# Kernel optimization log

Measured on AMD Instinct MI355X. Metric: run time of the kernel, lower is better.

The kernel has to match this reference:

```python
import jax, jax.numpy as jnp
import numpy as np

SIGMA_LIST = [0.05, 0.1, 0.2]
WEIGHT_LIST = [0.3, 0.3, 0.4]


def setup_inputs() -> dict:
    key = jax.random.key(0)
    k1, k2, k3 = jax.random.split(key, 3)
    B, N, M, D, C = 1, 8192, 8192, 3, 16
    x = jax.random.uniform(k1, (B, N, D), dtype=jnp.float32)
    y = jax.random.uniform(k2, (B, M, D), dtype=jnp.float32)
    y_fea = jax.random.normal(k3, (B, M, C), dtype=jnp.float32)
    return {"x": x, "y": y, "y_fea": y_fea}


def reference(x, y, y_fea):
    x2 = jnp.sum(x * x, axis=-1)  # [B, N]
    y2 = jnp.sum(y * y, axis=-1)  # [B, M]
    xy = jnp.einsum("bnd,bmd->bnm", x, y)  # [B, N, M]
    d2 = jnp.maximum(x2[:, :, None] + y2[:, None, :] - 2.0 * xy, 0.0)
    out = jnp.zeros(x.shape[:2] + (y_fea.shape[-1],), dtype=y_fea.dtype)
    for sigma, w in zip(SIGMA_LIST, WEIGHT_LIST):
        k = jnp.exp(d2 * (-1.0 / (2.0 * sigma * sigma)))  # [B, N, M]
        k = k / jnp.sum(k, axis=-1, keepdims=True)  # row-normalize over neighbors
        out = out + w * jnp.einsum("bnm,bmc->bnc", k, y_fea)
    return out
```

## Files before the change

kernel.cpp:

```cpp
#include <hip/hip_runtime.h>


static constexpr int Nn = 8192;
static constexpr int Mm = 8192;
static constexpr int NCH = 8;
static constexpr int NKT = 256 / NCH;
static constexpr float KC = 36.0673761f;
static constexpr float KD = -18.0336880f;

typedef _Float16 half8 __attribute__((ext_vector_type(8)));
typedef __fp16  fp16x2 __attribute__((ext_vector_type(2)));
typedef float  float4v __attribute__((ext_vector_type(4)));

#define MFMA_F16 __builtin_amdgcn_mfma_f32_16x16x32_f16
#define EXP2F(v) __builtin_amdgcn_exp2f(v)

__global__ __launch_bounds__(256) void mgsc_prep(
    const float* __restrict__ y, const float* __restrict__ yf,
    float4* __restrict__ q, _Float16* __restrict__ frag)
{
    const int t = blockIdx.x * 256 + threadIdx.x;
    const int m = t >> 4, c = t & 15;
    const int idx = ((m >> 5) << 9) + ((((m & 31) >> 3) << 4) + c) * 8 + (m & 7);
    frag[idx] = (_Float16)yf[t];
    if (t < Mm) {
        const float ax = y[3 * t], ay = y[3 * t + 1], az = y[3 * t + 2];
        q[t] = make_float4(KC * ax, KC * ay, KC * az,
                           KD * (ax * ax + ay * ay + az * az));
    }
}

__global__ __launch_bounds__(256, 4) void mgsc_main(
    const float* __restrict__ x, const float4* __restrict__ q,
    const _Float16* __restrict__ frag, float* __restrict__ part)
{
    __shared__ float4 qS[NKT * 32];

    const int tid  = threadIdx.x;
    const int wave = tid >> 6, lane = tid & 63;
    const int g    = lane >> 4, c = lane & 15;
    const int xb   = blockIdx.x, yb = blockIdx.y;
    const int n0   = (xb * 4 + wave) * 16;
    const int nrow = n0 + c;

    const float4* qsrc = q + ((size_t)yb * NKT << 5);
#pragma unroll
    for (int i = 0; i < NKT * 32 / 256; ++i)
        qS[tid + 256 * i] = qsrc[tid + 256 * i];

    const float xx = x[3 * nrow], xy = x[3 * nrow + 1], xz = x[3 * nrow + 2];
    const float E2x = EXP2F(KD * __fmaf_rn(xx, xx, __fmaf_rn(xy, xy, xz * xz)));

    float4v acc0 = {0.f, 0.f, 0.f, 0.f}, acc1 = acc0, acc2 = acc0;
    float4v dac0 = acc0, dac1 = acc0, dac2 = acc0;

    const _Float16 onev = (c == 0) ? (_Float16)1.0f : (_Float16)0.0f;
    half8 bone = {onev, onev, onev, onev, onev, onev, onev, onev};

    __syncthreads();

    const _Float16* fp = frag + ((size_t)yb * NKT << 9) + (lane << 3);
    half8 Bc = *reinterpret_cast<const half8*>(fp);

    for (int ktl = 0; ktl < NKT; ++ktl) {
        half8 Bn;
        if (ktl + 1 < NKT) {
            fp += 512;
            Bn = *reinterpret_cast<const half8*>(fp);
        }
        const float4* qk = &qS[(ktl << 5) + (g << 3)];
        float E2[8];
#pragma unroll
        for (int j = 0; j < 8; ++j) {
            const float4 Q = qk[j];
            const float arg = __fmaf_rn(xx, Q.x,
                              __fmaf_rn(xy, Q.y,
                              __fmaf_rn(xz, Q.z, Q.w)));
            E2[j] = E2x * EXP2F(arg);
        }
        union { fp16x2 h2[4]; half8 v; } A2, A1, A0;
#pragma unroll
        for (int jj = 0; jj < 4; ++jj) {
            A2.h2[jj] = __builtin_amdgcn_cvt_pkrtz(E2[2 * jj], E2[2 * jj + 1]);
            const fp16x2 s2 = A2.h2[jj] * A2.h2[jj];
            A1.h2[jj] = s2 * s2;
            const fp16x2 s1 = A1.h2[jj] * A1.h2[jj];
            A0.h2[jj] = s1 * s1;
        }
        acc0 = MFMA_F16(A0.v, Bc, acc0, 0, 0, 0);
        acc1 = MFMA_F16(A1.v, Bc, acc1, 0, 0, 0);
        acc2 = MFMA_F16(A2.v, Bc, acc2, 0, 0, 0);
        dac0 = MFMA_F16(A0.v, bone, dac0, 0, 0, 0);
        dac1 = MFMA_F16(A1.v, bone, dac1, 0, 0, 0);
        dac2 = MFMA_F16(A2.v, bone, dac2, 0, 0, 0);
        if (ktl + 1 < NKT) Bc = Bn;
    }

    float* pb = part + ((size_t)yb * Nn) * 52;
#pragma unroll
    for (int r = 0; r < 4; ++r) {
        const int n = n0 + (g << 2) + r;
        float* row = pb + (size_t)n * 52;
        row[c]      = acc0[r];
        row[16 + c] = acc1[r];
        row[32 + c] = acc2[r];
        if (c == 0) {
            row[48] = dac0[r];
            row[49] = dac1[r];
            row[50] = dac2[r];
        }
    }
}

__global__ __launch_bounds__(256) void mgsc_reduce(
    const float* __restrict__ part, float* __restrict__ out)
{
    const int t = blockIdx.x * 256 + threadIdx.x;
    const int n = t >> 4, c = t & 15;
    float s0 = 0.f, s1 = 0.f, s2 = 0.f, d0 = 0.f, d1 = 0.f, d2 = 0.f;
#pragma unroll
    for (int k = 0; k < NCH; ++k) {
        const float* row = part + ((size_t)k * Nn + n) * 52;
        s0 += row[c];
        s1 += row[16 + c];
        s2 += row[32 + c];
        d0 += row[48];
        d1 += row[49];
        d2 += row[50];
    }
    out[(size_t)n * 16 + c] = 0.3f * s0 / d0 + 0.3f * s1 / d1 + 0.4f * s2 / d2;
}

__global__ __launch_bounds__(256) void mgsc_fused(
    const float* __restrict__ x, const float* __restrict__ y,
    const float* __restrict__ yf, float* __restrict__ out)
{
    __shared__ float yS[256 * 3];
    __shared__ float yfS[256 * 16];
    const int tid = threadIdx.x;
    const int n   = blockIdx.x * 256 + tid;
    const float xx = x[3 * n], xy = x[3 * n + 1], xz = x[3 * n + 2];
    float a0[16], a1[16], a2[16];
#pragma unroll
    for (int c = 0; c < 16; ++c) { a0[c] = 0.f; a1[c] = 0.f; a2[c] = 0.f; }
    float den0 = 0.f, den1 = 0.f, den2 = 0.f;
    for (int mt = 0; mt < Mm; mt += 256) {
        const float4* ysrc = reinterpret_cast<const float4*>(y + (size_t)mt * 3);
        if (tid < 192) reinterpret_cast<float4*>(yS)[tid] = ysrc[tid];
        const float4* fsrc = reinterpret_cast<const float4*>(yf + (size_t)mt * 16);
#pragma unroll
        for (int k = 0; k < 4; ++k)
            reinterpret_cast<float4*>(yfS)[tid + 256 * k] = fsrc[tid + 256 * k];
        __syncthreads();
        for (int mm = 0; mm < 256; ++mm) {
            const float dx = xx - yS[3 * mm], dy = xy - yS[3 * mm + 1], dz = xz - yS[3 * mm + 2];
            const float d2 = dx * dx + dy * dy + dz * dz;
            const float e2 = __expf(-12.5f * d2);
            const float t = e2 * e2, e1 = t * t, u = e1 * e1, e0 = u * u;
            den0 += e0; den1 += e1; den2 += e2;
            const float4* fr = reinterpret_cast<const float4*>(yfS + mm * 16);
#pragma unroll
            for (int k = 0; k < 4; ++k) {
                const float4 f = fr[k];
                a0[4*k+0] += e0 * f.x; a0[4*k+1] += e0 * f.y; a0[4*k+2] += e0 * f.z; a0[4*k+3] += e0 * f.w;
                a1[4*k+0] += e1 * f.x; a1[4*k+1] += e1 * f.y; a1[4*k+2] += e1 * f.z; a1[4*k+3] += e1 * f.w;
                a2[4*k+0] += e2 * f.x; a2[4*k+1] += e2 * f.y; a2[4*k+2] += e2 * f.z; a2[4*k+3] += e2 * f.w;
            }
        }
        __syncthreads();
    }
    const float r0 = 0.3f / den0, r1 = 0.3f / den1, r2 = 0.4f / den2;
#pragma unroll
    for (int c = 0; c < 16; ++c)
        out[(size_t)n * 16 + c] = a0[c] * r0 + a1[c] * r1 + a2[c] * r2;
}

extern "C" void kernel_launch(void* const* d_in, const int* in_sizes, int n_in,
                              void* d_out, int out_size, void* d_ws, size_t ws_size,
                              hipStream_t stream) {
    const float* x  = (const float*)d_in[0];
    const float* y  = (const float*)d_in[1];
    const float* yf = (const float*)d_in[2];
    float* out = (float*)d_out;

    const size_t qB    = (size_t)Mm * sizeof(float4);
    const size_t fragB = (size_t)Mm * 16 * sizeof(_Float16);
    const size_t partB = (size_t)NCH * Nn * 52 * sizeof(float);
    if (qB + fragB + partB > ws_size) {
        mgsc_fused<<<Nn / 256, 256, 0, stream>>>(x, y, yf, out);
        return;
    }
    float4*   q    = (float4*)d_ws;
    _Float16* frag = (_Float16*)((char*)d_ws + qB);
    float*    part = (float*)((char*)d_ws + qB + fragB);

    mgsc_prep<<<(Mm * 16) / 256, 256, 0, stream>>>(y, yf, q, frag);
    mgsc_main<<<dim3(Nn / 64, NCH), 256, 0, stream>>>(x, q, frag, part);
    mgsc_reduce<<<(Nn * 16) / 256, 256, 0, stream>>>(part, out);
}
```

Before: 88.66 us.

## Process two 16-row tiles per wave to reuse B fragments, double M-chunks

Each wave now computes two 16-row x tiles (32 rows), so each loaded y_fea fragment and each LDS q read feed twice as many MFMAs and exp evaluations. The grid is halved along N and the number of M-chunks (NCH) is doubled to 16, which keeps the block count about the same and halves the K length per block. Costs: twice the accumulator registers, which may lower occupancy, and twice the partial-sum buffer that the reduce kernel must read.

```diff
diff --git a/kernel.cpp b/kernel.cpp
--- a/kernel.cpp
+++ b/kernel.cpp
@@ -3,13 +3,15 @@
 
 static constexpr int Nn = 8192;
 static constexpr int Mm = 8192;
-static constexpr int NCH = 8;
+static constexpr int NCH = 16;
 static constexpr int NKT = 256 / NCH;
 static constexpr float KC = 36.0673761f;
 static constexpr float KD = -18.0336880f;
 
 typedef _Float16 half8 __attribute__((ext_vector_type(8)));
 typedef __fp16  fp16x2 __attribute__((ext_vector_type(2)));
+typedef __fp16  fp16x4 __attribute__((ext_vector_type(4)));
+typedef __fp16  fp16x8 __attribute__((ext_vector_type(8)));
 typedef float  float4v __attribute__((ext_vector_type(4)));
 
 #define MFMA_F16 __builtin_amdgcn_mfma_f32_16x16x32_f16
@@ -30,6 +32,36 @@
     }
 }
 
+struct Frags { half8 a0, a1, a2; };
+__device__ __forceinline__ Frags make_frags(const float E[8]) {
+    fp16x2 p[4], q1[4], q0[4];
+#pragma unroll
+    for (int jj = 0; jj < 4; ++jj) {
+        p[jj] = __builtin_amdgcn_cvt_pkrtz(E[2 * jj], E[2 * jj + 1]);
+        const fp16x2 s2 = p[jj] * p[jj];
+        q1[jj] = s2 * s2;
+        const fp16x2 s1 = q1[jj] * q1[jj];
+        q0[jj] = s1 * s1;
+    }
+    Frags f;
+    {
+        const fp16x4 lo = __builtin_shufflevector(p[0], p[1], 0, 1, 2, 3);
+        const fp16x4 hi = __builtin_shufflevector(p[2], p[3], 0, 1, 2, 3);
+        f.a2 = __builtin_bit_cast(half8, __builtin_shufflevector(lo, hi, 0, 1, 2, 3, 4, 5, 6, 7));
+    }
+    {
+        const fp16x4 lo = __builtin_shufflevector(q1[0], q1[1], 0, 1, 2, 3);
+        const fp16x4 hi = __builtin_shufflevector(q1[2], q1[3], 0, 1, 2, 3);
+        f.a1 = __builtin_bit_cast(half8, __builtin_shufflevector(lo, hi, 0, 1, 2, 3, 4, 5, 6, 7));
+    }
+    {
+        const fp16x4 lo = __builtin_shufflevector(q0[0], q0[1], 0, 1, 2, 3);
+        const fp16x4 hi = __builtin_shufflevector(q0[2], q0[3], 0, 1, 2, 3);
+        f.a0 = __builtin_bit_cast(half8, __builtin_shufflevector(lo, hi, 0, 1, 2, 3, 4, 5, 6, 7));
+    }
+    return f;
+}
+
 __global__ __launch_bounds__(256, 4) void mgsc_main(
     const float* __restrict__ x, const float4* __restrict__ q,
     const _Float16* __restrict__ frag, float* __restrict__ part)
@@ -40,75 +72,80 @@
     const int wave = tid >> 6, lane = tid & 63;
     const int g    = lane >> 4, c = lane & 15;
     const int xb   = blockIdx.x, yb = blockIdx.y;
-    const int n0   = (xb * 4 + wave) * 16;
-    const int nrow = n0 + c;
+    const int n0   = (xb * 4 + wave) * 32;
+    const int rA   = n0 + c;
+    const int rB   = n0 + 16 + c;
 
     const float4* qsrc = q + ((size_t)yb * NKT << 5);
-#pragma unroll
-    for (int i = 0; i < NKT * 32 / 256; ++i)
-        qS[tid + 256 * i] = qsrc[tid + 256 * i];
-
-    const float xx = x[3 * nrow], xy = x[3 * nrow + 1], xz = x[3 * nrow + 2];
-    const float E2x = EXP2F(KD * __fmaf_rn(xx, xx, __fmaf_rn(xy, xy, xz * xz)));
-
-    float4v acc0 = {0.f, 0.f, 0.f, 0.f}, acc1 = acc0, acc2 = acc0;
-    float4v dac0 = acc0, dac1 = acc0, dac2 = acc0;
+    qS[tid]       = qsrc[tid];
+    qS[tid + 256] = qsrc[tid + 256];
+
+    const float xxA = x[3 * rA], xyA = x[3 * rA + 1], xzA = x[3 * rA + 2];
+    const float xxB = x[3 * rB], xyB = x[3 * rB + 1], xzB = x[3 * rB + 2];
+    const float E2xA = EXP2F(KD * __fmaf_rn(xxA, xxA, __fmaf_rn(xyA, xyA, xzA * xzA)));
+    const float E2xB = EXP2F(KD * __fmaf_rn(xxB, xxB, __fmaf_rn(xyB, xyB, xzB * xzB)));
+
+    float4v aA0 = {0.f, 0.f, 0.f, 0.f}, aA1 = aA0, aA2 = aA0;
+    float4v dA0 = aA0, dA1 = aA0, dA2 = aA0;
+    float4v aB0 = aA0, aB1 = aA0, aB2 = aA0;
+    float4v dB0 = aA0, dB1 = aA0, dB2 = aA0;
 
     const _Float16 onev = (c == 0) ? (_Float16)1.0f : (_Float16)0.0f;
     half8 bone = {onev, onev, onev, onev, onev, onev, onev, onev};
 
     __syncthreads();
 
-    const _Float16* fp = frag + ((size_t)yb * NKT << 9) + (lane << 3);
-    half8 Bc = *reinterpret_cast<const half8*>(fp);
+    const _Float16* fpp = frag + ((size_t)yb * NKT << 9) + (lane << 3);
+    half8 Bc = *reinterpret_cast<const half8*>(fpp);
 
     for (int ktl = 0; ktl < NKT; ++ktl) {
         half8 Bn;
         if (ktl + 1 < NKT) {
-            fp += 512;
-            Bn = *reinterpret_cast<const half8*>(fp);
+            fpp += 512;
+            Bn = *reinterpret_cast<const half8*>(fpp);
         }
         const float4* qk = &qS[(ktl << 5) + (g << 3)];
-        float E2[8];
+        float EA[8], EB[8];
 #pragma unroll
         for (int j = 0; j < 8; ++j) {
             const float4 Q = qk[j];
-            const float arg = __fmaf_rn(xx, Q.x,
-                              __fmaf_rn(xy, Q.y,
-                              __fmaf_rn(xz, Q.z, Q.w)));
-            E2[j] = E2x * EXP2F(arg);
+            const float argA = __fmaf_rn(xxA, Q.x, __fmaf_rn(xyA, Q.y, __fmaf_rn(xzA, Q.z, Q.w)));
+            const float argB = __fmaf_rn(xxB, Q.x, __fmaf_rn(xyB, Q.y, __fmaf_rn(xzB, Q.z, Q.w)));
+            EA[j] = E2xA * EXP2F(argA);
+            EB[j] = E2xB * EXP2F(argB);
         }
-        union { fp16x2 h2[4]; half8 v; } A2, A1, A0;
-#pragma unroll
-        for (int jj = 0; jj < 4; ++jj) {
-            A2.h2[jj] = __builtin_amdgcn_cvt_pkrtz(E2[2 * jj], E2[2 * jj + 1]);
-            const fp16x2 s2 = A2.h2[jj] * A2.h2[jj];
-            A1.h2[jj] = s2 * s2;
-            const fp16x2 s1 = A1.h2[jj] * A1.h2[jj];
-            A0.h2[jj] = s1 * s1;
-        }
-        acc0 = MFMA_F16(A0.v, Bc, acc0, 0, 0, 0);
-        acc1 = MFMA_F16(A1.v, Bc, acc1, 0, 0, 0);
-        acc2 = MFMA_F16(A2.v, Bc, acc2, 0, 0, 0);
-        dac0 = MFMA_F16(A0.v, bone, dac0, 0, 0, 0);
-        dac1 = MFMA_F16(A1.v, bone, dac1, 0, 0, 0);
-        dac2 = MFMA_F16(A2.v, bone, dac2, 0, 0, 0);
+        const Frags fA = make_frags(EA);
+        const Frags fB = make_frags(EB);
+        aA0 = MFMA_F16(fA.a0, Bc, aA0, 0, 0, 0);
+        aA1 = MFMA_F16(fA.a1, Bc, aA1, 0, 0, 0);
+        aA2 = MFMA_F16(fA.a2, Bc, aA2, 0, 0, 0);
+        dA0 = MFMA_F16(fA.a0, bone, dA0, 0, 0, 0);
+        dA1 = MFMA_F16(fA.a1, bone, dA1, 0, 0, 0);
+        dA2 = MFMA_F16(fA.a2, bone, dA2, 0, 0, 0);
+        aB0 = MFMA_F16(fB.a0, Bc, aB0, 0, 0, 0);
+        aB1 = MFMA_F16(fB.a1, Bc, aB1, 0, 0, 0);
+        aB2 = MFMA_F16(fB.a2, Bc, aB2, 0, 0, 0);
+        dB0 = MFMA_F16(fB.a0, bone, dB0, 0, 0, 0);
+        dB1 = MFMA_F16(fB.a1, bone, dB1, 0, 0, 0);
+        dB2 = MFMA_F16(fB.a2, bone, dB2, 0, 0, 0);
         if (ktl + 1 < NKT) Bc = Bn;
     }
 
     float* pb = part + ((size_t)yb * Nn) * 52;
 #pragma unroll
     for (int r = 0; r < 4; ++r) {
-        const int n = n0 + (g << 2) + r;
-        float* row = pb + (size_t)n * 52;
-        row[c]      = acc0[r];
-        row[16 + c] = acc1[r];
-        row[32 + c] = acc2[r];
-        if (c == 0) {
-            row[48] = dac0[r];
-            row[49] = dac1[r];
-            row[50] = dac2[r];
-        }
+        const int nA = n0 + (g << 2) + r;
+        float* rowA = pb + (size_t)nA * 52;
+        rowA[c]      = aA0[r];
+        rowA[16 + c] = aA1[r];
+        rowA[32 + c] = aA2[r];
+        if (c == 0) { rowA[48] = dA0[r]; rowA[49] = dA1[r]; rowA[50] = dA2[r]; }
+        const int nB = n0 + 16 + (g << 2) + r;
+        float* rowB = pb + (size_t)nB * 52;
+        rowB[c]      = aB0[r];
+        rowB[16 + c] = aB1[r];
+        rowB[32 + c] = aB2[r];
+        if (c == 0) { rowB[48] = dB0[r]; rowB[49] = dB1[r]; rowB[50] = dB2[r]; }
     }
 }
 
@@ -195,6 +232,6 @@
     float*    part = (float*)((char*)d_ws + qB + fragB);
 
     mgsc_prep<<<(Mm * 16) / 256, 256, 0, stream>>>(y, yf, q, frag);
-    mgsc_main<<<dim3(Nn / 64, NCH), 256, 0, stream>>>(x, q, frag, part);
+    mgsc_main<<<dim3(Nn / 128, NCH), 256, 0, stream>>>(x, q, frag, part);
     mgsc_reduce<<<(Nn * 16) / 256, 256, 0, stream>>>(part, out);
 }
```

Result: slower. 93.43 us (+5.4%).

## Fuse prep kernel into main by staging y and features into LDS per block

Applied to the files above, without the earlier changes.

Removes the separate prep launch. Each main block now computes its own scaled y coordinates (stored structure-of-arrays in LDS) and converts its chunk of features to fp16 MFMA fragment layout in LDS. The B operand is then read from LDS each iteration instead of being prefetched from global memory. This saves one kernel launch and a global round trip. In exchange, every one of the 128 x-blocks redoes the conversion of the same y chunk, LDS usage rises, and the launch-bounds occupancy hint is dropped.

```diff
diff --git a/kernel.cpp b/kernel.cpp
--- a/kernel.cpp
+++ b/kernel.cpp
@@ -4,7 +4,8 @@
 static constexpr int Nn = 8192;
 static constexpr int Mm = 8192;
 static constexpr int NCH = 8;
-static constexpr int NKT = 256 / NCH;
+static constexpr int MC  = Mm / NCH;
+static constexpr int NKT = MC / 32;
 static constexpr float KC = 36.0673761f;
 static constexpr float KD = -18.0336880f;
 
@@ -15,26 +16,12 @@
 #define MFMA_F16 __builtin_amdgcn_mfma_f32_16x16x32_f16
 #define EXP2F(v) __builtin_amdgcn_exp2f(v)
 
-__global__ __launch_bounds__(256) void mgsc_prep(
-    const float* __restrict__ y, const float* __restrict__ yf,
-    float4* __restrict__ q, _Float16* __restrict__ frag)
+__global__ __launch_bounds__(256) void mgsc_main(
+    const float* __restrict__ x, const float* __restrict__ y,
+    const float* __restrict__ yf, float* __restrict__ part)
 {
-    const int t = blockIdx.x * 256 + threadIdx.x;
-    const int m = t >> 4, c = t & 15;
-    const int idx = ((m >> 5) << 9) + ((((m & 31) >> 3) << 4) + c) * 8 + (m & 7);
-    frag[idx] = (_Float16)yf[t];
-    if (t < Mm) {
-        const float ax = y[3 * t], ay = y[3 * t + 1], az = y[3 * t + 2];
-        q[t] = make_float4(KC * ax, KC * ay, KC * az,
-                           KD * (ax * ax + ay * ay + az * az));
-    }
-}
-
-__global__ __launch_bounds__(256, 4) void mgsc_main(
-    const float* __restrict__ x, const float4* __restrict__ q,
-    const _Float16* __restrict__ frag, float* __restrict__ part)
-{
-    __shared__ float4 qS[NKT * 32];
+    __shared__ float    qS[4][MC];
+    __shared__ _Float16 fragS[MC * 16];
 
     const int tid  = threadIdx.x;
     const int wave = tid >> 6, lane = tid & 63;
@@ -42,11 +29,30 @@
     const int xb   = blockIdx.x, yb = blockIdx.y;
     const int n0   = (xb * 4 + wave) * 16;
     const int nrow = n0 + c;
-
-    const float4* qsrc = q + ((size_t)yb * NKT << 5);
-#pragma unroll
-    for (int i = 0; i < NKT * 32 / 256; ++i)
-        qS[tid + 256 * i] = qsrc[tid + 256 * i];
+    const int m0   = yb * MC;
+
+#pragma unroll
+    for (int i = 0; i < 4; ++i) {
+        const int ml = tid + i * 256;
+        const int gm = m0 + ml;
+        const float ax = y[3 * gm], ay = y[3 * gm + 1], az = y[3 * gm + 2];
+        qS[0][ml] = KC * ax;
+        qS[1][ml] = KC * ay;
+        qS[2][ml] = KC * az;
+        qS[3][ml] = KD * __fmaf_rn(ax, ax, __fmaf_rn(ay, ay, az * az));
+    }
+    const float4* fsrc = reinterpret_cast<const float4*>(yf + (size_t)m0 * 16);
+#pragma unroll
+    for (int i = 0; i < 16; ++i) {
+        const int idx = tid + i * 256;
+        const int ml = idx >> 2, c0 = (idx & 3) << 2;
+        const float4 v = fsrc[idx];
+        _Float16* dst = fragS + ((ml >> 5) << 9) + ((((ml & 31) >> 3) << 4) + c0) * 8 + (ml & 7);
+        dst[0]  = (_Float16)v.x;
+        dst[8]  = (_Float16)v.y;
+        dst[16] = (_Float16)v.z;
+        dst[24] = (_Float16)v.w;
+    }
 
     const float xx = x[3 * nrow], xy = x[3 * nrow + 1], xz = x[3 * nrow + 2];
     const float E2x = EXP2F(KD * __fmaf_rn(xx, xx, __fmaf_rn(xy, xy, xz * xz)));
@@ -59,23 +65,26 @@
 
     __syncthreads();
 
-    const _Float16* fp = frag + ((size_t)yb * NKT << 9) + (lane << 3);
-    half8 Bc = *reinterpret_cast<const half8*>(fp);
-
     for (int ktl = 0; ktl < NKT; ++ktl) {
-        half8 Bn;
-        if (ktl + 1 < NKT) {
-            fp += 512;
-            Bn = *reinterpret_cast<const half8*>(fp);
-        }
-        const float4* qk = &qS[(ktl << 5) + (g << 3)];
+        const int qb = (ktl << 5) + (g << 3);
+        const float4v X0 = *reinterpret_cast<const float4v*>(&qS[0][qb]);
+        const float4v X1 = *reinterpret_cast<const float4v*>(&qS[0][qb + 4]);
+        const float4v Y0 = *reinterpret_cast<const float4v*>(&qS[1][qb]);
+        const float4v Y1 = *reinterpret_cast<const float4v*>(&qS[1][qb + 4]);
+        const float4v Z0 = *reinterpret_cast<const float4v*>(&qS[2][qb]);
+        const float4v Z1 = *reinterpret_cast<const float4v*>(&qS[2][qb + 4]);
+        const float4v W0 = *reinterpret_cast<const float4v*>(&qS[3][qb]);
+        const float4v W1 = *reinterpret_cast<const float4v*>(&qS[3][qb + 4]);
+        const float W = KD * 0.f;
+        (void)W;
         float E2[8];
 #pragma unroll
         for (int j = 0; j < 8; ++j) {
-            const float4 Q = qk[j];
-            const float arg = __fmaf_rn(xx, Q.x,
-                              __fmaf_rn(xy, Q.y,
-                              __fmaf_rn(xz, Q.z, Q.w)));
+            const float Qx = (j < 4) ? X0[j & 3] : X1[j & 3];
+            const float Qy = (j < 4) ? Y0[j & 3] : Y1[j & 3];
+            const float Qz = (j < 4) ? Z0[j & 3] : Z1[j & 3];
+            const float Qw = (j < 4) ? W0[j & 3] : W1[j & 3];
+            const float arg = __fmaf_rn(xx, Qx, __fmaf_rn(xy, Qy, __fmaf_rn(xz, Qz, Qw)));
             E2[j] = E2x * EXP2F(arg);
         }
         union { fp16x2 h2[4]; half8 v; } A2, A1, A0;
@@ -87,13 +96,13 @@
             const fp16x2 s1 = A1.h2[jj] * A1.h2[jj];
             A0.h2[jj] = s1 * s1;
         }
-        acc0 = MFMA_F16(A0.v, Bc, acc0, 0, 0, 0);
-        acc1 = MFMA_F16(A1.v, Bc, acc1, 0, 0, 0);
-        acc2 = MFMA_F16(A2.v, Bc, acc2, 0, 0, 0);
+        const half8 B = *reinterpret_cast<const half8*>(fragS + (ktl << 9) + (lane << 3));
+        acc0 = MFMA_F16(A0.v, B, acc0, 0, 0, 0);
+        acc1 = MFMA_F16(A1.v, B, acc1, 0, 0, 0);
+        acc2 = MFMA_F16(A2.v, B, acc2, 0, 0, 0);
         dac0 = MFMA_F16(A0.v, bone, dac0, 0, 0, 0);
         dac1 = MFMA_F16(A1.v, bone, dac1, 0, 0, 0);
         dac2 = MFMA_F16(A2.v, bone, dac2, 0, 0, 0);
-        if (ktl + 1 < NKT) Bc = Bn;
     }
 
     float* pb = part + ((size_t)yb * Nn) * 52;
@@ -183,18 +192,13 @@
     const float* yf = (const float*)d_in[2];
     float* out = (float*)d_out;
 
-    const size_t qB    = (size_t)Mm * sizeof(float4);
-    const size_t fragB = (size_t)Mm * 16 * sizeof(_Float16);
     const size_t partB = (size_t)NCH * Nn * 52 * sizeof(float);
-    if (qB + fragB + partB > ws_size) {
+    if (partB > ws_size) {
         mgsc_fused<<<Nn / 256, 256, 0, stream>>>(x, y, yf, out);
         return;
     }
-    float4*   q    = (float4*)d_ws;
-    _Float16* frag = (_Float16*)((char*)d_ws + qB);
-    float*    part = (float*)((char*)d_ws + qB + fragB);
-
-    mgsc_prep<<<(Mm * 16) / 256, 256, 0, stream>>>(y, yf, q, frag);
-    mgsc_main<<<dim3(Nn / 64, NCH), 256, 0, stream>>>(x, q, frag, part);
+    float* part = (float*)d_ws;
+
+    mgsc_main<<<dim3(Nn / 64, NCH), 256, 0, stream>>>(x, y, yf, part);
     mgsc_reduce<<<(Nn * 16) / 256, 256, 0, stream>>>(part, out);
 }
```

Result: slower. 92.59 us (+4.4%).
